# Kernel tuning notes

Measured on AMD Instinct MI355X. Metric: run time of the kernel, lower is better.

The kernel has to match this reference:

```python
import jax, jax.numpy as jnp
import numpy as np

N_NODES = 50000
N_EDGES = 800000
N_GRAPHS = 128
D_IN, D_HID, D_OUT = 128, 128, 128  # gnn_input_dim, gnn_hidden_dim, gnn_output_dim
EPS = 1e-5
NEG_SLOPE = 0.01


def setup_inputs() -> dict:
    key = jax.random.key(0)
    ks = jax.random.split(key, 16)
    x = jax.random.normal(ks[0], (N_NODES, D_IN), jnp.float32)
    edge_index = jax.random.randint(ks[1], (2, N_EDGES), 0, N_NODES, dtype=jnp.int64)
    batch = jnp.sort(jax.random.randint(ks[2], (N_NODES,), 0, N_GRAPHS, dtype=jnp.int64))

    def lin(k, fi, fo):
        return jax.random.normal(k, (fi, fo), jnp.float32) * (1.0 / np.sqrt(fi))

    d2, d4 = 2 * D_HID, 4 * D_HID
    return {
        "x": x, "edge_index": edge_index, "batch": batch, "batch_size": N_GRAPHS,
        "W1": lin(ks[3], D_IN, d2), "b1": jnp.zeros((d2,), jnp.float32),
        "g1": jnp.ones((d2,), jnp.float32), "be1": jnp.zeros((d2,), jnp.float32),
        "W2": lin(ks[4], d2, d4), "b2": jnp.zeros((d4,), jnp.float32),
        "g2": jnp.ones((d4,), jnp.float32), "be2": jnp.zeros((d4,), jnp.float32),
        "W3": lin(ks[5], d4, d4), "b3": jnp.zeros((d4,), jnp.float32),
        "g3": jnp.ones((d4,), jnp.float32), "be3": jnp.zeros((d4,), jnp.float32),
        "Wf": lin(ks[6], d4, D_OUT), "bf": jnp.zeros((D_OUT,), jnp.float32),
    }


def _layernorm(h, g, b):
    mu = jnp.mean(h, axis=-1, keepdims=True)
    var = jnp.mean(jnp.square(h - mu), axis=-1, keepdims=True)
    return (h - mu) * jax.lax.rsqrt(var + EPS) * g + b


def _gcn_conv(h, W, b, src, dst, norm, n):
    # h' = D^-1/2 (A+I) D^-1/2 (h W) + b   (PyG GCNConv with self-loops)
    m = h @ W                                    # [N, F_out]
    msg = m[src] * norm[:, None]                 # [E+N, F_out]
    return jax.ops.segment_sum(msg, dst, num_segments=n) + b


def reference(x, edge_index, batch, batch_size, W1, b1, g1, be1,
              W2, b2, g2, be2, W3, b3, g3, be3, Wf, bf):
    n = x.shape[0]
    loop = jnp.arange(n, dtype=edge_index.dtype)
    src = jnp.concatenate([edge_index[0], loop])
    dst = jnp.concatenate([edge_index[1], loop])
    deg = jax.ops.segment_sum(jnp.ones_like(dst, dtype=x.dtype), dst, num_segments=n)
    dinv = jax.lax.rsqrt(deg)                    # deg >= 1 due to self loops
    norm = dinv[src] * dinv[dst]

    h = _gcn_conv(x, W1, b1, src, dst, norm, n)
    h = jax.nn.leaky_relu(_layernorm(h, g1, be1), NEG_SLOPE)
    h = _gcn_conv(h, W2, b2, src, dst, norm, n)
    h = jax.nn.leaky_relu(_layernorm(h, g2, be2), NEG_SLOPE)
    h = _gcn_conv(h, W3, b3, src, dst, norm, n)
    h = _layernorm(h, g3, be3)

    # global average pool per graph
    sums = jax.ops.segment_sum(h, batch, num_segments=batch_size)
    cnt = jax.ops.segment_sum(jnp.ones((n,), h.dtype), batch, num_segments=batch_size)
    pooled = sums / jnp.maximum(cnt, 1.0)[:, None]
    return pooled @ Wf + bf
```

## Files before the change

### kernel.cpp

```cpp
#include <hip/hip_runtime.h>
#include <hip/hip_bf16.h>
#include <math.h>

#define GRAPHS 128
#define SCAN_B 256
#define BM 128
#define BN 128
#define BK 64
#define PCH 128

typedef __attribute__((ext_vector_type(8))) short bfrag8;
typedef __attribute__((ext_vector_type(4))) float f32x4;

__device__ inline unsigned short f2b(float f) {
    unsigned int u = __float_as_uint(f);
    unsigned int r = (u + 0x7fffu + ((u >> 16) & 1u)) >> 16;
    return (unsigned short)r;
}
__device__ inline float b2f(unsigned short u) {
    return __uint_as_float(((unsigned int)u) << 16);
}
__device__ inline void unpack8(float* v, uint4 u) {
    v[0] = b2f(u.x & 0xffffu); v[1] = b2f(u.x >> 16);
    v[2] = b2f(u.y & 0xffffu); v[3] = b2f(u.y >> 16);
    v[4] = b2f(u.z & 0xffffu); v[5] = b2f(u.z >> 16);
    v[6] = b2f(u.w & 0xffffu); v[7] = b2f(u.w >> 16);
}

__device__ inline void gload16(const void* g, void* l) {
    typedef unsigned int __attribute__((address_space(1))) gu32;
    typedef unsigned int __attribute__((address_space(3))) su32;
    __builtin_amdgcn_global_load_lds((const gu32*)g, (su32*)l, 16, 0, 0);
}

__device__ inline int xcd_vid(int p, int nwg) {
    int q = nwg >> 3, r = nwg & 7, x = p & 7, ix = p >> 3;
    return (x < r ? x * (q + 1) : r * (q + 1) + (x - r) * q) + ix;
}


__global__ void k_count(const int* __restrict__ dst, int* __restrict__ cnt, int E) {
    int i = blockIdx.x * blockDim.x + threadIdx.x;
    if (i < E) atomicAdd(&cnt[dst[i]], 1);
}

__global__ void k_scan1(const int* __restrict__ cnt, int* __restrict__ excl,
                        int* __restrict__ bsum, int n) {
    __shared__ int sh[SCAN_B];
    int t = threadIdx.x;
    int i = blockIdx.x * SCAN_B + t;
    int v = (i < n) ? cnt[i] : 0;
    sh[t] = v;
    __syncthreads();
    for (int off = 1; off < SCAN_B; off <<= 1) {
        int x = (t >= off) ? sh[t - off] : 0;
        __syncthreads();
        sh[t] += x;
        __syncthreads();
    }
    if (i < n) excl[i] = sh[t] - v;
    if (t == SCAN_B - 1) bsum[blockIdx.x] = sh[t];
}

__global__ void k_scan2(int* __restrict__ bsum, int nb) {
    __shared__ int sh[SCAN_B];
    int t = threadIdx.x;
    int v = (t < nb) ? bsum[t] : 0;
    sh[t] = v;
    __syncthreads();
    for (int off = 1; off < SCAN_B; off <<= 1) {
        int x = (t >= off) ? sh[t - off] : 0;
        __syncthreads();
        sh[t] += x;
        __syncthreads();
    }
    if (t < nb) bsum[t] = sh[t] - v;
}

__global__ void k_scan3(int* __restrict__ rowstart, const int* __restrict__ bsum,
                        const int* __restrict__ cnt, float* __restrict__ dinv,
                        int* __restrict__ cursor, int n, int E) {
    int i = blockIdx.x * SCAN_B + threadIdx.x;
    if (i < n) {
        rowstart[i] += bsum[blockIdx.x];
        cursor[i] = 0;
        dinv[i] = rsqrtf((float)cnt[i] + 1.0f);
    }
    if (i == 0) rowstart[n] = E;
}

__global__ void k_scatter_csr(const int* __restrict__ src, const int* __restrict__ dst,
                              const float* __restrict__ dinv, const int* __restrict__ rowstart,
                              int* __restrict__ cursor, int2* __restrict__ csr, int E) {
    int e = blockIdx.x * blockDim.x + threadIdx.x;
    if (e >= E) return;
    int s = src[e], d = dst[e];
    int pos = rowstart[d] + atomicAdd(&cursor[d], 1);
    int2 c;
    c.x = s;
    c.y = __float_as_int(dinv[s] * dinv[d]);
    csr[pos] = c;
}


__global__ void k_wt(const float* __restrict__ W, unsigned short* __restrict__ WT,
                     int K, int N) {
    int idx = blockIdx.x * 256 + threadIdx.x;
    if (idx >= K * N) return;
    int k = idx / N, n2 = idx - k * N;
    WT[(size_t)n2 * K + k] = f2b(W[idx]);
}


__global__ void k_x2b(const float* __restrict__ x, unsigned short* __restrict__ xb,
                      int n, int mpad) {
    int idx = blockIdx.x * 256 + threadIdx.x;
    if (idx >= mpad * 32) return;
    int row = idx >> 5;
    float4 v = {0.f, 0.f, 0.f, 0.f};
    if (row < n) v = ((const float4*)x)[idx];
    ushort4 o;
    o.x = f2b(v.x); o.y = f2b(v.y); o.z = f2b(v.z); o.w = f2b(v.w);
    ((ushort4*)xb)[idx] = o;
}


__device__ inline void acc8(float* a, uint4 u, float w) {
    a[0] += b2f(u.x & 0xffffu) * w; a[1] += b2f(u.x >> 16) * w;
    a[2] += b2f(u.y & 0xffffu) * w; a[3] += b2f(u.y >> 16) * w;
    a[4] += b2f(u.z & 0xffffu) * w; a[5] += b2f(u.z >> 16) * w;
    a[6] += b2f(u.w & 0xffffu) * w; a[7] += b2f(u.w >> 16) * w;
}

template <int F>
__global__ void k_aggb(const unsigned short* __restrict__ m, unsigned short* __restrict__ agg,
                       const int* __restrict__ rowstart, const int2* __restrict__ csr,
                       const float* __restrict__ dinv, int n, int mpad) {
    constexpr int TPN = F / 8;
    constexpr int NPB = 256 / TPN;
    int node = blockIdx.x * NPB + (int)(threadIdx.x / TPN);
    int fo = (int)(threadIdx.x % TPN) * 8;
    if (node >= mpad) return;
    uint4* dst = (uint4*)(agg + (size_t)node * F + fo);
    if (node >= n) { uint4 z = {0u, 0u, 0u, 0u}; *dst = z; return; }

    const unsigned short* mf = m + fo;
    float di = dinv[node];
    float a[8] = {};
    acc8(a, *(const uint4*)(mf + (size_t)node * F), di * di);

    int b = rowstart[node], e = rowstart[node + 1];
    int j = b;
    for (; j + 4 <= e; j += 4) {
        int2 c0 = csr[j], c1 = csr[j + 1], c2 = csr[j + 2], c3 = csr[j + 3];
        uint4 u0 = *(const uint4*)(mf + (size_t)c0.x * F);
        uint4 u1 = *(const uint4*)(mf + (size_t)c1.x * F);
        uint4 u2 = *(const uint4*)(mf + (size_t)c2.x * F);
        uint4 u3 = *(const uint4*)(mf + (size_t)c3.x * F);
        acc8(a, u0, __int_as_float(c0.y));
        acc8(a, u1, __int_as_float(c1.y));
        acc8(a, u2, __int_as_float(c2.y));
        acc8(a, u3, __int_as_float(c3.y));
    }
    for (; j < e; ++j) {
        int2 c = csr[j];
        uint4 u = *(const uint4*)(mf + (size_t)c.x * F);
        acc8(a, u, __int_as_float(c.y));
    }
    uint4 o;
    o.x = (unsigned)f2b(a[0]) | ((unsigned)f2b(a[1]) << 16);
    o.y = (unsigned)f2b(a[2]) | ((unsigned)f2b(a[3]) << 16);
    o.z = (unsigned)f2b(a[4]) | ((unsigned)f2b(a[5]) << 16);
    o.w = (unsigned)f2b(a[6]) | ((unsigned)f2b(a[7]) << 16);
    *dst = o;
}


__device__ inline void acc8i(float* a, uint2 u, float w) {
    a[0] += (float)(signed char)(u.x) * w;
    a[1] += (float)(signed char)(u.x >> 8) * w;
    a[2] += (float)(signed char)(u.x >> 16) * w;
    a[3] += (float)(signed char)(u.x >> 24) * w;
    a[4] += (float)(signed char)(u.y) * w;
    a[5] += (float)(signed char)(u.y >> 8) * w;
    a[6] += (float)(signed char)(u.y >> 16) * w;
    a[7] += (float)(signed char)(u.y >> 24) * w;
}

template <int F>
__global__ void k_agg8(const signed char* __restrict__ q8, const float* __restrict__ scale,
                       unsigned short* __restrict__ agg, const int* __restrict__ rowstart,
                       const int2* __restrict__ csr, const float* __restrict__ dinv,
                       int n, int mpad) {
    constexpr int TPN = F / 8;
    constexpr int NPB = 256 / TPN;
    int node = blockIdx.x * NPB + (int)(threadIdx.x / TPN);
    int fo = (int)(threadIdx.x % TPN) * 8;
    if (node >= mpad) return;
    uint4* dst = (uint4*)(agg + (size_t)node * F + fo);
    if (node >= n) { uint4 z = {0u, 0u, 0u, 0u}; *dst = z; return; }

    const signed char* qf = q8 + fo;
    float di = dinv[node];
    float a[8] = {};
    {
        uint2 u = *(const uint2*)(qf + (size_t)node * F);
        acc8i(a, u, di * di * scale[node]);
    }
    int b = rowstart[node], e = rowstart[node + 1];
    int j = b;
    for (; j + 2 <= e; j += 2) {
        int2 c0 = csr[j], c1 = csr[j + 1];
        uint2 u0 = *(const uint2*)(qf + (size_t)c0.x * F);
        uint2 u1 = *(const uint2*)(qf + (size_t)c1.x * F);
        float w0 = __int_as_float(c0.y) * scale[c0.x];
        float w1 = __int_as_float(c1.y) * scale[c1.x];
        acc8i(a, u0, w0);
        acc8i(a, u1, w1);
    }
    for (; j < e; ++j) {
        int2 c = csr[j];
        uint2 u = *(const uint2*)(qf + (size_t)c.x * F);
        acc8i(a, u, __int_as_float(c.y) * scale[c.x]);
    }
    uint4 o;
    o.x = (unsigned)f2b(a[0]) | ((unsigned)f2b(a[1]) << 16);
    o.y = (unsigned)f2b(a[2]) | ((unsigned)f2b(a[3]) << 16);
    o.z = (unsigned)f2b(a[4]) | ((unsigned)f2b(a[5]) << 16);
    o.w = (unsigned)f2b(a[6]) | ((unsigned)f2b(a[7]) << 16);
    *dst = o;
}


__global__ __launch_bounds__(256) void k_gemm_bf16(
    const unsigned short* __restrict__ A, const unsigned short* __restrict__ BT,
    const float* __restrict__ bias, unsigned short* __restrict__ C,
    int K, int N, int ncb) {
    __shared__ __align__(16) char sA[BM * BK * 2];
    __shared__ __align__(16) char sB[BN * BK * 2];

    const int vid = xcd_vid((int)blockIdx.x, (int)gridDim.x);
    const int rb = vid / ncb;
    const int cb = vid - rb * ncb;
    const int tid = threadIdx.x;
    const int lane = tid & 63;
    const int wave = tid >> 6;
    const int wr = wave >> 1, wc = wave & 1;
    const size_t row0 = (size_t)rb * BM;
    const size_t col0 = (size_t)cb * BN;

    const unsigned short* srcA[4];
    const unsigned short* srcB[4];
    char* dstA[4];
    char* dstB[4];
#pragma unroll
    for (int c = 0; c < 4; ++c) {
        int idx = c * 256 + tid;
        int row = idx >> 3;
        int cbl = ((idx & 7) << 4) ^ ((row & 7) << 4);
        srcA[c] = A + (row0 + row) * K + (cbl >> 1);
        srcB[c] = BT + (col0 + row) * K + (cbl >> 1);
        dstA[c] = sA + idx * 16;
        dstB[c] = sB + idx * 16;
    }

    const int fr = lane & 15;
    const int fg = lane >> 4;
    const int fsw = (lane & 7) << 4;
    int offA[4][2], offB[4][2];
#pragma unroll
    for (int t = 0; t < 4; ++t)
#pragma unroll
        for (int kk = 0; kk < 2; ++kk) {
            offA[t][kk] = (wr * 64 + t * 16 + fr) * (BK * 2) + ((kk * 64 + fg * 16) ^ fsw);
            offB[t][kk] = (wc * 64 + t * 16 + fr) * (BK * 2) + ((kk * 64 + fg * 16) ^ fsw);
        }

    f32x4 acc[4][4] = {};

    for (int k0 = 0; k0 < K; k0 += BK) {
#pragma unroll
        for (int c = 0; c < 4; ++c) gload16(srcA[c] + k0, dstA[c]);
#pragma unroll
        for (int c = 0; c < 4; ++c) gload16(srcB[c] + k0, dstB[c]);
        __syncthreads();
#pragma unroll
        for (int kk = 0; kk < 2; ++kk) {
            bfrag8 av[4], bv[4];
#pragma unroll
            for (int t = 0; t < 4; ++t) av[t] = *(const bfrag8*)(sA + offA[t][kk]);
#pragma unroll
            for (int t = 0; t < 4; ++t) bv[t] = *(const bfrag8*)(sB + offB[t][kk]);
#pragma unroll
            for (int i = 0; i < 4; ++i)
#pragma unroll
                for (int j = 0; j < 4; ++j)
                    acc[i][j] = __builtin_amdgcn_mfma_f32_16x16x32_bf16(av[i], bv[j],
                                                                        acc[i][j], 0, 0, 0);
        }
        __syncthreads();
    }

#pragma unroll
    for (int i = 0; i < 4; ++i) {
#pragma unroll
        for (int j = 0; j < 4; ++j) {
            size_t r = row0 + wr * 64 + i * 16 + fg * 4;
            size_t cc = col0 + wc * 64 + j * 16 + fr;
            float bb = bias[cc];
#pragma unroll
            for (int q = 0; q < 4; ++q)
                C[(r + q) * N + cc] = f2b(acc[i][j][q] + bb);
        }
    }
}


template <int F, bool LRELU>
__global__ void k_lnr8(const unsigned short* __restrict__ z, signed char* __restrict__ q8,
                       float* __restrict__ scale, const float* __restrict__ g,
                       const float* __restrict__ be, int mpad) {
    constexpr int V = F / 64;
    int row = blockIdx.x * 4 + (threadIdx.x >> 6);
    int lane = threadIdx.x & 63;
    const unsigned short* p = z + (size_t)row * F + lane * V;
    float v[V];
    if constexpr (V == 8) {
        uint4 u = *(const uint4*)p;
        unpack8(v, u);
    } else {
        uint2 u = *(const uint2*)p;
        v[0] = b2f(u.x & 0xffffu); v[1] = b2f(u.x >> 16);
        v[2] = b2f(u.y & 0xffffu); v[3] = b2f(u.y >> 16);
    }
    float s = 0.f, q = 0.f;
#pragma unroll
    for (int k = 0; k < V; ++k) { s += v[k]; q += v[k] * v[k]; }
#pragma unroll
    for (int m = 1; m < 64; m <<= 1) {
        s += __shfl_xor(s, m);
        q += __shfl_xor(q, m);
    }
    float mu = s * (1.0f / F);
    float var = q * (1.0f / F) - mu * mu;
    float rs = rsqrtf(var + 1e-5f);

    float y[V];
    float mx = 0.f;
#pragma unroll
    for (int k = 0; k < V; ++k) {
        float yy = (v[k] - mu) * rs * g[lane * V + k] + be[lane * V + k];
        if (LRELU) yy = fmaxf(yy, 0.f) + 0.01f * fminf(yy, 0.f);
        y[k] = yy;
        mx = fmaxf(mx, fabsf(yy));
    }
#pragma unroll
    for (int m = 1; m < 64; m <<= 1) mx = fmaxf(mx, __shfl_xor(mx, m));

    float inv = (mx > 0.f) ? 127.0f / mx : 0.f;
    unsigned int ob[V / 4];
#pragma unroll
    for (int k = 0; k < V; k += 4) {
        int q0 = __float2int_rn(y[k] * inv);
        int q1 = __float2int_rn(y[k + 1] * inv);
        int q2 = __float2int_rn(y[k + 2] * inv);
        int q3 = __float2int_rn(y[k + 3] * inv);
        ob[k / 4] = (q0 & 0xff) | ((q1 & 0xff) << 8) | ((q2 & 0xff) << 16) | ((q3 & 0xff) << 24);
    }
    signed char* qp = q8 + (size_t)row * F + lane * V;
    if constexpr (V == 8) *(uint2*)qp = *(uint2*)ob;
    else                  *(unsigned int*)qp = ob[0];
    if (lane == 0) scale[row] = mx * (1.0f / 127.0f);
}


template <int F>
__global__ void k_stats(const unsigned short* __restrict__ z, float2* __restrict__ st,
                        int mpad) {
    int row = blockIdx.x * 4 + (threadIdx.x >> 6);
    int lane = threadIdx.x & 63;
    const unsigned short* p = z + (size_t)row * F + lane * 8;
    uint4 u = *(const uint4*)p;
    float v[8]; unpack8(v, u);
    float s = 0.f, q = 0.f;
#pragma unroll
    for (int k = 0; k < 8; ++k) { s += v[k]; q += v[k] * v[k]; }
#pragma unroll
    for (int m = 1; m < 64; m <<= 1) {
        s += __shfl_xor(s, m);
        q += __shfl_xor(q, m);
    }
    if (lane == 0) {
        float mu = s * (1.0f / F);
        float var = q * (1.0f / F) - mu * mu;
        float2 o; o.x = mu; o.y = rsqrtf(var + 1e-5f);
        st[row] = o;
    }
}


__global__ void k_pool3(const unsigned short* __restrict__ z, const float2* __restrict__ st,
                        const float* __restrict__ g, const float* __restrict__ be,
                        const int* __restrict__ batch, float* __restrict__ pooled, int n) {
    int i0 = blockIdx.x * PCH;
    int iend = i0 + PCH; if (iend > n) iend = n;
    int t = threadIdx.x;
    float g0 = g[t * 2], g1 = g[t * 2 + 1];
    float e0 = be[t * 2], e1 = be[t * 2 + 1];
    float s0 = 0.f, s1 = 0.f;
    int cur = batch[i0];
    for (int i = i0; i < iend; ++i) {
        int gg = batch[i];
        if (gg != cur) {
            atomicAdd(&pooled[(size_t)cur * 512 + t * 2], s0);
            atomicAdd(&pooled[(size_t)cur * 512 + t * 2 + 1], s1);
            s0 = s1 = 0.f;
            cur = gg;
        }
        float2 s2 = st[i];
        unsigned int u = *(const unsigned int*)(z + (size_t)i * 512 + t * 2);
        s0 += (b2f(u & 0xffffu) - s2.x) * s2.y * g0 + e0;
        s1 += (b2f(u >> 16) - s2.x) * s2.y * g1 + e1;
    }
    atomicAdd(&pooled[(size_t)cur * 512 + t * 2], s0);
    atomicAdd(&pooled[(size_t)cur * 512 + t * 2 + 1], s1);
}


__global__ void k_final(const float* __restrict__ pooled, const int* __restrict__ batch,
                        const float* __restrict__ Wf, const float* __restrict__ bf,
                        float* __restrict__ out, int n) {
    int gph = blockIdx.x;
    int o = threadIdx.x;
    int lo = 0, hi = n;
    while (lo < hi) { int mid = (lo + hi) >> 1; if (batch[mid] < gph) lo = mid + 1; else hi = mid; }
    int start = lo;
    lo = start; hi = n;
    while (lo < hi) { int mid = (lo + hi) >> 1; if (batch[mid] < gph + 1) lo = mid + 1; else hi = mid; }
    int end = lo;
    float inv = 1.0f / fmaxf((float)(end - start), 1.0f);

    __shared__ float p[512];
    for (int k = threadIdx.x; k < 512; k += 128) p[k] = pooled[(size_t)gph * 512 + k] * inv;
    __syncthreads();
    float acc = bf[o];
#pragma unroll 8
    for (int k = 0; k < 512; ++k) acc += p[k] * Wf[(size_t)k * 128 + o];
    out[(size_t)gph * 128 + o] = acc;
}


static inline size_t align_up(size_t x) { return (x + 255) & ~(size_t)255; }

extern "C" void kernel_launch(void* const* d_in, const int* in_sizes, int n_in,
                              void* d_out, int out_size, void* d_ws, size_t ws_size,
                              hipStream_t stream) {
    const float* x     = (const float*)d_in[0];
    const int*   ei    = (const int*)d_in[1];
    const int*   batch = (const int*)d_in[2];
    const float* W1 = (const float*)d_in[4],  *b1 = (const float*)d_in[5];
    const float* g1 = (const float*)d_in[6],  *be1= (const float*)d_in[7];
    const float* W2 = (const float*)d_in[8],  *b2 = (const float*)d_in[9];
    const float* g2 = (const float*)d_in[10], *be2= (const float*)d_in[11];
    const float* W3 = (const float*)d_in[12], *b3 = (const float*)d_in[13];
    const float* g3 = (const float*)d_in[14], *be3= (const float*)d_in[15];
    const float* Wf = (const float*)d_in[16], *bf = (const float*)d_in[17];
    float* out = (float*)d_out;

    const int N = in_sizes[0] / 128;
    const int E = in_sizes[1] / 2;
    const int Mpad = ((N + BM - 1) / BM) * BM;
    const int* src = ei;
    const int* dst = ei + E;

    char* ws = (char*)d_ws;
    size_t off = 0;
    auto take = [&](size_t bytes) { char* p = ws + off; off += align_up(bytes); return p; };

    unsigned short* zb      = (unsigned short*)take((size_t)Mpad * 512 * 2);
    unsigned short* aggb    = (unsigned short*)take((size_t)Mpad * 512 * 2);
    signed char*    q8      = (signed char*)take((size_t)Mpad * 512);
    float*          scale   = (float*)take((size_t)Mpad * 4);
    unsigned short* xb      = (unsigned short*)take((size_t)Mpad * 128 * 2);
    unsigned short* wt1     = (unsigned short*)take((size_t)256 * 128 * 2);
    unsigned short* wt2     = (unsigned short*)take((size_t)512 * 256 * 2);
    unsigned short* wt3     = (unsigned short*)take((size_t)512 * 512 * 2);
    float2*         st      = (float2*)take((size_t)Mpad * 8);
    float*          dinv    = (float*)take((size_t)N * 4);
    int*            rowstart= (int*)  take((size_t)(N + 1) * 4);
    int*            cnt     = (int*)  take((size_t)N * 4);
    int*            cursor  = (int*)  take((size_t)N * 4);
    int*            bsum    = (int*)  take((size_t)SCAN_B * 4);
    int2*           csr     = (int2*) take((size_t)E * 8);
    float*          pooled  = (float*)take((size_t)GRAPHS * 512 * 4);

    const int nb = (N + SCAN_B - 1) / SCAN_B;
    const int NR4 = Mpad / 4;

    hipMemsetAsync(cnt, 0, (size_t)N * 4, stream);
    k_count<<<(E + 255) / 256, 256, 0, stream>>>(dst, cnt, E);
    k_scan1<<<nb, SCAN_B, 0, stream>>>(cnt, rowstart, bsum, N);
    k_scan2<<<1, SCAN_B, 0, stream>>>(bsum, nb);
    k_scan3<<<nb, SCAN_B, 0, stream>>>(rowstart, bsum, cnt, dinv, cursor, N, E);
    k_scatter_csr<<<(E + 255) / 256, 256, 0, stream>>>(src, dst, dinv, rowstart, cursor, csr, E);

    k_wt<<<(128 * 256 + 255) / 256, 256, 0, stream>>>(W1, wt1, 128, 256);
    k_wt<<<(256 * 512 + 255) / 256, 256, 0, stream>>>(W2, wt2, 256, 512);
    k_wt<<<(512 * 512 + 255) / 256, 256, 0, stream>>>(W3, wt3, 512, 512);

    k_x2b<<<(Mpad * 32 + 255) / 256, 256, 0, stream>>>(x, xb, N, Mpad);

    k_aggb<128><<<Mpad / 16, 256, 0, stream>>>(xb, aggb, rowstart, csr, dinv, N, Mpad);
    k_gemm_bf16<<<(Mpad / BM) * 2, 256, 0, stream>>>(aggb, wt1, b1, zb, 128, 256, 2);
    k_lnr8<256, true><<<NR4, 256, 0, stream>>>(zb, q8, scale, g1, be1, Mpad);

    k_agg8<256><<<Mpad / 8, 256, 0, stream>>>(q8, scale, aggb, rowstart, csr, dinv, N, Mpad);
    k_gemm_bf16<<<(Mpad / BM) * 4, 256, 0, stream>>>(aggb, wt2, b2, zb, 256, 512, 4);
    k_lnr8<512, true><<<NR4, 256, 0, stream>>>(zb, q8, scale, g2, be2, Mpad);

    k_agg8<512><<<Mpad / 4, 256, 0, stream>>>(q8, scale, aggb, rowstart, csr, dinv, N, Mpad);
    k_gemm_bf16<<<(Mpad / BM) * 4, 256, 0, stream>>>(aggb, wt3, b3, zb, 512, 512, 4);
    k_stats<512><<<NR4, 256, 0, stream>>>(zb, st, Mpad);

    hipMemsetAsync(pooled, 0, (size_t)GRAPHS * 512 * 4, stream);
    k_pool3<<<(N + PCH - 1) / PCH, 256, 0, stream>>>(zb, st, g3, be3, batch, pooled, N);
    k_final<<<GRAPHS, 128, 0, stream>>>(pooled, batch, Wf, bf, out, N);
}
```

Baseline: 442.0 us.

## Quantize input to int8, fuse final LayerNorm stats into pooling, merge weight transposes

Three launches for the weight transposes become one. The input features are now quantized per row to int8 with a scale, so the first aggregation uses the int8 gather kernel, which moves half the bytes of the bf16 gather. The separate stats kernel for the last LayerNorm is removed: the pool kernel computes each row's mean and variance with wave shuffles and normalizes in place, saving one full pass over the 512-wide activations. The int8 input quantization adds precision loss on the raw input features.

```diff
diff --git a/kernel.cpp b/kernel.cpp
--- a/kernel.cpp
+++ b/kernel.cpp
@@ -103,76 +103,38 @@
 }
 
 
-__global__ void k_wt(const float* __restrict__ W, unsigned short* __restrict__ WT,
-                     int K, int N) {
+__global__ void k_wt3(const float* __restrict__ W1, const float* __restrict__ W2,
+                      const float* __restrict__ W3, unsigned short* __restrict__ T1,
+                      unsigned short* __restrict__ T2, unsigned short* __restrict__ T3) {
     int idx = blockIdx.x * 256 + threadIdx.x;
-    if (idx >= K * N) return;
+    const float* W; unsigned short* T; int K, N;
+    if (idx < 32768) { W = W1; T = T1; K = 128; N = 256; }
+    else if (idx < 163840) { idx -= 32768; W = W2; T = T2; K = 256; N = 512; }
+    else { idx -= 163840; if (idx >= 262144) return; W = W3; T = T3; K = 512; N = 512; }
     int k = idx / N, n2 = idx - k * N;
-    WT[(size_t)n2 * K + k] = f2b(W[idx]);
-}
-
-
-__global__ void k_x2b(const float* __restrict__ x, unsigned short* __restrict__ xb,
-                      int n, int mpad) {
-    int idx = blockIdx.x * 256 + threadIdx.x;
-    if (idx >= mpad * 32) return;
-    int row = idx >> 5;
-    float4 v = {0.f, 0.f, 0.f, 0.f};
-    if (row < n) v = ((const float4*)x)[idx];
-    ushort4 o;
-    o.x = f2b(v.x); o.y = f2b(v.y); o.z = f2b(v.z); o.w = f2b(v.w);
-    ((ushort4*)xb)[idx] = o;
-}
-
-
-__device__ inline void acc8(float* a, uint4 u, float w) {
-    a[0] += b2f(u.x & 0xffffu) * w; a[1] += b2f(u.x >> 16) * w;
-    a[2] += b2f(u.y & 0xffffu) * w; a[3] += b2f(u.y >> 16) * w;
-    a[4] += b2f(u.z & 0xffffu) * w; a[5] += b2f(u.z >> 16) * w;
-    a[6] += b2f(u.w & 0xffffu) * w; a[7] += b2f(u.w >> 16) * w;
-}
-
-template <int F>
-__global__ void k_aggb(const unsigned short* __restrict__ m, unsigned short* __restrict__ agg,
-                       const int* __restrict__ rowstart, const int2* __restrict__ csr,
-                       const float* __restrict__ dinv, int n, int mpad) {
-    constexpr int TPN = F / 8;
-    constexpr int NPB = 256 / TPN;
-    int node = blockIdx.x * NPB + (int)(threadIdx.x / TPN);
-    int fo = (int)(threadIdx.x % TPN) * 8;
-    if (node >= mpad) return;
-    uint4* dst = (uint4*)(agg + (size_t)node * F + fo);
-    if (node >= n) { uint4 z = {0u, 0u, 0u, 0u}; *dst = z; return; }
-
-    const unsigned short* mf = m + fo;
-    float di = dinv[node];
-    float a[8] = {};
-    acc8(a, *(const uint4*)(mf + (size_t)node * F), di * di);
-
-    int b = rowstart[node], e = rowstart[node + 1];
-    int j = b;
-    for (; j + 4 <= e; j += 4) {
-        int2 c0 = csr[j], c1 = csr[j + 1], c2 = csr[j + 2], c3 = csr[j + 3];
-        uint4 u0 = *(const uint4*)(mf + (size_t)c0.x * F);
-        uint4 u1 = *(const uint4*)(mf + (size_t)c1.x * F);
-        uint4 u2 = *(const uint4*)(mf + (size_t)c2.x * F);
-        uint4 u3 = *(const uint4*)(mf + (size_t)c3.x * F);
-        acc8(a, u0, __int_as_float(c0.y));
-        acc8(a, u1, __int_as_float(c1.y));
-        acc8(a, u2, __int_as_float(c2.y));
-        acc8(a, u3, __int_as_float(c3.y));
-    }
-    for (; j < e; ++j) {
-        int2 c = csr[j];
-        uint4 u = *(const uint4*)(mf + (size_t)c.x * F);
-        acc8(a, u, __int_as_float(c.y));
-    }
-    uint4 o;
-    o.x = (unsigned)f2b(a[0]) | ((unsigned)f2b(a[1]) << 16);
-    o.y = (unsigned)f2b(a[2]) | ((unsigned)f2b(a[3]) << 16);
-    o.z = (unsigned)f2b(a[4]) | ((unsigned)f2b(a[5]) << 16);
-    o.w = (unsigned)f2b(a[6]) | ((unsigned)f2b(a[7]) << 16);
-    *dst = o;
+    T[(size_t)n2 * K + k] = f2b(W[idx]);
+}
+
+
+__global__ void k_x2q(const float* __restrict__ x, signed char* __restrict__ q,
+                      float* __restrict__ sc, int n, int mpad) {
+    int row = blockIdx.x * 4 + (threadIdx.x >> 6);
+    int lane = threadIdx.x & 63;
+    if (row >= mpad) return;
+    signed char* qp = q + (size_t)row * 128 + lane * 2;
+    if (row >= n) {
+        *(unsigned short*)qp = 0;
+        if (lane == 0) sc[row] = 0.f;
+        return;
+    }
+    float2 v = *(const float2*)(x + (size_t)row * 128 + lane * 2);
+    float mx = fmaxf(fabsf(v.x), fabsf(v.y));
+#pragma unroll
+    for (int m = 1; m < 64; m <<= 1) mx = fmaxf(mx, __shfl_xor(mx, m));
+    float inv = (mx > 0.f) ? 127.0f / mx : 0.f;
+    int q0 = __float2int_rn(v.x * inv), q1 = __float2int_rn(v.y * inv);
+    *(unsigned short*)qp = (unsigned short)((q0 & 0xff) | ((q1 & 0xff) << 8));
+    if (lane == 0) sc[row] = mx * (1.0f / 127.0f);
 }
 
 
@@ -374,56 +336,57 @@
 }
 
 
-template <int F>
-__global__ void k_stats(const unsigned short* __restrict__ z, float2* __restrict__ st,
-                        int mpad) {
-    int row = blockIdx.x * 4 + (threadIdx.x >> 6);
-    int lane = threadIdx.x & 63;
-    const unsigned short* p = z + (size_t)row * F + lane * 8;
-    uint4 u = *(const uint4*)p;
-    float v[8]; unpack8(v, u);
-    float s = 0.f, q = 0.f;
-#pragma unroll
-    for (int k = 0; k < 8; ++k) { s += v[k]; q += v[k] * v[k]; }
-#pragma unroll
-    for (int m = 1; m < 64; m <<= 1) {
-        s += __shfl_xor(s, m);
-        q += __shfl_xor(q, m);
-    }
-    if (lane == 0) {
-        float mu = s * (1.0f / F);
-        float var = q * (1.0f / F) - mu * mu;
-        float2 o; o.x = mu; o.y = rsqrtf(var + 1e-5f);
-        st[row] = o;
-    }
-}
-
-
-__global__ void k_pool3(const unsigned short* __restrict__ z, const float2* __restrict__ st,
-                        const float* __restrict__ g, const float* __restrict__ be,
-                        const int* __restrict__ batch, float* __restrict__ pooled, int n) {
+__global__ void k_pool4(const unsigned short* __restrict__ z, const float* __restrict__ g,
+                        const float* __restrict__ be, const int* __restrict__ batch,
+                        float* __restrict__ pooled, int n) {
     int i0 = blockIdx.x * PCH;
     int iend = i0 + PCH; if (iend > n) iend = n;
-    int t = threadIdx.x;
-    float g0 = g[t * 2], g1 = g[t * 2 + 1];
-    float e0 = be[t * 2], e1 = be[t * 2 + 1];
-    float s0 = 0.f, s1 = 0.f;
-    int cur = batch[i0];
-    for (int i = i0; i < iend; ++i) {
+    int w = threadIdx.x >> 6, lane = threadIdx.x & 63;
+    int f0 = lane * 8;
+    float gk[8], ek[8];
+    {
+        float4 ga = *(const float4*)(g + f0), gb = *(const float4*)(g + f0 + 4);
+        float4 ea = *(const float4*)(be + f0), eb = *(const float4*)(be + f0 + 4);
+        gk[0] = ga.x; gk[1] = ga.y; gk[2] = ga.z; gk[3] = ga.w;
+        gk[4] = gb.x; gk[5] = gb.y; gk[6] = gb.z; gk[7] = gb.w;
+        ek[0] = ea.x; ek[1] = ea.y; ek[2] = ea.z; ek[3] = ea.w;
+        ek[4] = eb.x; ek[5] = eb.y; ek[6] = eb.z; ek[7] = eb.w;
+    }
+    float a[8] = {};
+    int cur = -1;
+    for (int i = i0 + w; i < iend; i += 4) {
         int gg = batch[i];
         if (gg != cur) {
-            atomicAdd(&pooled[(size_t)cur * 512 + t * 2], s0);
-            atomicAdd(&pooled[(size_t)cur * 512 + t * 2 + 1], s1);
-            s0 = s1 = 0.f;
+            if (cur >= 0) {
+                float* pp = pooled + (size_t)cur * 512 + f0;
+#pragma unroll
+                for (int k = 0; k < 8; ++k) atomicAdd(&pp[k], a[k]);
+            }
+#pragma unroll
+            for (int k = 0; k < 8; ++k) a[k] = 0.f;
             cur = gg;
         }
-        float2 s2 = st[i];
-        unsigned int u = *(const unsigned int*)(z + (size_t)i * 512 + t * 2);
-        s0 += (b2f(u & 0xffffu) - s2.x) * s2.y * g0 + e0;
-        s1 += (b2f(u >> 16) - s2.x) * s2.y * g1 + e1;
-    }
-    atomicAdd(&pooled[(size_t)cur * 512 + t * 2], s0);
-    atomicAdd(&pooled[(size_t)cur * 512 + t * 2 + 1], s1);
+        uint4 u = *(const uint4*)(z + (size_t)i * 512 + f0);
+        float v[8]; unpack8(v, u);
+        float s = 0.f, q = 0.f;
+#pragma unroll
+        for (int k = 0; k < 8; ++k) { s += v[k]; q += v[k] * v[k]; }
+#pragma unroll
+        for (int m = 1; m < 64; m <<= 1) {
+            s += __shfl_xor(s, m);
+            q += __shfl_xor(q, m);
+        }
+        float mu = s * (1.0f / 512.0f);
+        float var = q * (1.0f / 512.0f) - mu * mu;
+        float rs = rsqrtf(var + 1e-5f);
+#pragma unroll
+        for (int k = 0; k < 8; ++k) a[k] += (v[k] - mu) * rs * gk[k] + ek[k];
+    }
+    if (cur >= 0) {
+        float* pp = pooled + (size_t)cur * 512 + f0;
+#pragma unroll
+        for (int k = 0; k < 8; ++k) atomicAdd(&pp[k], a[k]);
+    }
 }
 
 
@@ -481,11 +444,11 @@
     unsigned short* aggb    = (unsigned short*)take((size_t)Mpad * 512 * 2);
     signed char*    q8      = (signed char*)take((size_t)Mpad * 512);
     float*          scale   = (float*)take((size_t)Mpad * 4);
-    unsigned short* xb      = (unsigned short*)take((size_t)Mpad * 128 * 2);
+    signed char*    q8x     = (signed char*)take((size_t)Mpad * 128);
+    float*          sx      = (float*)take((size_t)Mpad * 4);
     unsigned short* wt1     = (unsigned short*)take((size_t)256 * 128 * 2);
     unsigned short* wt2     = (unsigned short*)take((size_t)512 * 256 * 2);
     unsigned short* wt3     = (unsigned short*)take((size_t)512 * 512 * 2);
-    float2*         st      = (float2*)take((size_t)Mpad * 8);
     float*          dinv    = (float*)take((size_t)N * 4);
     int*            rowstart= (int*)  take((size_t)(N + 1) * 4);
     int*            cnt     = (int*)  take((size_t)N * 4);
@@ -504,13 +467,11 @@
     k_scan3<<<nb, SCAN_B, 0, stream>>>(rowstart, bsum, cnt, dinv, cursor, N, E);
     k_scatter_csr<<<(E + 255) / 256, 256, 0, stream>>>(src, dst, dinv, rowstart, cursor, csr, E);
 
-    k_wt<<<(128 * 256 + 255) / 256, 256, 0, stream>>>(W1, wt1, 128, 256);
-    k_wt<<<(256 * 512 + 255) / 256, 256, 0, stream>>>(W2, wt2, 256, 512);
-    k_wt<<<(512 * 512 + 255) / 256, 256, 0, stream>>>(W3, wt3, 512, 512);
-
-    k_x2b<<<(Mpad * 32 + 255) / 256, 256, 0, stream>>>(x, xb, N, Mpad);
-
-    k_aggb<128><<<Mpad / 16, 256, 0, stream>>>(xb, aggb, rowstart, csr, dinv, N, Mpad);
+    k_wt3<<<(425984 + 255) / 256, 256, 0, stream>>>(W1, W2, W3, wt1, wt2, wt3);
+
+    k_x2q<<<NR4, 256, 0, stream>>>(x, q8x, sx, N, Mpad);
+
+    k_agg8<128><<<Mpad / 16, 256, 0, stream>>>(q8x, sx, aggb, rowstart, csr, dinv, N, Mpad);
     k_gemm_bf16<<<(Mpad / BM) * 2, 256, 0, stream>>>(aggb, wt1, b1, zb, 128, 256, 2);
     k_lnr8<256, true><<<NR4, 256, 0, stream>>>(zb, q8, scale, g1, be1, Mpad);
 
@@ -520,9 +481,8 @@
 
     k_agg8<512><<<Mpad / 4, 256, 0, stream>>>(q8, scale, aggb, rowstart, csr, dinv, N, Mpad);
     k_gemm_bf16<<<(Mpad / BM) * 4, 256, 0, stream>>>(aggb, wt3, b3, zb, 512, 512, 4);
-    k_stats<512><<<NR4, 256, 0, stream>>>(zb, st, Mpad);
 
     hipMemsetAsync(pooled, 0, (size_t)GRAPHS * 512 * 4, stream);
-    k_pool3<<<(N + PCH - 1) / PCH, 256, 0, stream>>>(zb, st, g3, be3, batch, pooled, N);
+    k_pool4<<<(N + PCH - 1) / PCH, 256, 0, stream>>>(zb, g3, be3, batch, pooled, N);
     k_final<<<GRAPHS, 128, 0, stream>>>(pooled, batch, Wf, bf, out, N);
 }
```

New measurement: 437.1 us. Within noise of the previous version (-1.1%).
